# Kernel optimization log

Measured on AMD Instinct MI355X. Metric: run time of the kernel, lower is better.

## Reference

```python
import jax, jax.numpy as jnp
import numpy as np

H = 4096          # hidden_size
I = 2048          # moe_intermediate_size * n_shared_experts
SWIGLU_LIMIT = 10.0
QMAX = 127.0


def _quantize_weight(w):
    # per-output-channel symmetric int8 quantization of a float weight [out, in]
    s = jnp.maximum(jnp.max(jnp.abs(w), axis=1) / QMAX, 1e-8)      # [out]
    q = jnp.clip(jnp.round(w / s[:, None]), -QMAX, QMAX)           # int8-valued
    return q.astype(jnp.float32), s.astype(jnp.float32)


def setup_inputs() -> dict:
    key = jax.random.key(0)
    ks = jax.random.split(key, 4)
    x = jax.random.normal(ks[0], (2, 4096, H), dtype=jnp.float32)
    w_gate, s_wgate = _quantize_weight(jax.random.normal(ks[1], (I, H)) * 0.02)
    w_up, s_wup = _quantize_weight(jax.random.normal(ks[2], (I, H)) * 0.02)
    w_down, s_wdown = _quantize_weight(jax.random.normal(ks[3], (H, I)) * 0.02)
    inv_gate = jnp.ones((H,), jnp.float32)
    inv_up = jnp.ones((H,), jnp.float32)
    inv_inter = jnp.ones((I,), jnp.float32)
    return {"x": x, "w_gate": w_gate, "s_wgate": s_wgate, "w_up": w_up,
            "s_wup": s_wup, "w_down": w_down, "s_wdown": s_wdown,
            "inv_gate": inv_gate, "inv_up": inv_up, "inv_inter": inv_inter}


def _dynamic_quant(x, inv_smooth):
    # per-token symmetric int8 dynamic quant with smoothing scale
    xs = x.astype(jnp.float32) * inv_smooth                        # [T, D]
    scale = jnp.maximum(jnp.max(jnp.abs(xs), axis=-1, keepdims=True) / QMAX, 1e-8)
    q = jnp.clip(jnp.round(xs / scale), -QMAX, QMAX)
    return q, scale


def _quant_gemm(q, x_scale, w_q, w_scale):
    acc = q @ w_q.T                                                # fp32 accumulate
    return acc * x_scale * w_scale[None, :]


def reference(x, w_gate, s_wgate, w_up, s_wup, w_down, s_wdown,
              inv_gate, inv_up, inv_inter):
    orig_shape = x.shape
    x_flat = x.reshape(-1, H).astype(jnp.bfloat16)                 # [T, H]
    qg, sg = _dynamic_quant(x_flat, inv_gate)
    qu, su = _dynamic_quant(x_flat, inv_up)
    gate_out = _quant_gemm(qg, sg, w_gate, s_wgate)                # [T, I]
    up_out = _quant_gemm(qu, su, w_up, s_wup)                      # [T, I]
    inter = jax.nn.silu(gate_out) * up_out
    inter = jnp.clip(inter, -SWIGLU_LIMIT, SWIGLU_LIMIT).astype(jnp.bfloat16)
    qi, si = _dynamic_quant(inter, inv_inter)
    out = _quant_gemm(qi, si, w_down, s_wdown)                     # [T, H]
    return out.reshape(orig_shape)
```

## Files before the change

### kernel.cpp

```cpp
#include <hip/hip_runtime.h>
#include <hip/hip_bf16.h>


typedef __attribute__((ext_vector_type(4))) int i32x4;

__device__ __forceinline__ void async16(void* lds, const void* g) {
  __builtin_amdgcn_global_load_lds(
      (const __attribute__((address_space(1))) void*)g,
      (__attribute__((address_space(3))) void*)lds, 16, 0, 0);
}

__device__ __forceinline__ i32x4 mfma_i8(i32x4 a, i32x4 b, i32x4 c) {
  return __builtin_amdgcn_mfma_i32_16x16x64_i8(a, b, c, 0, 0, 0);
}

__device__ __forceinline__ float bf16_rne_f(float f) {
  unsigned u = __float_as_uint(f);
  u += 0x7fffu + ((u >> 16) & 1u);
  return __uint_as_float(u & 0xffff0000u);
}

__device__ __forceinline__ unsigned short bf16_bits(float f) {
  unsigned u = __float_as_uint(f);
  u += 0x7fffu + ((u >> 16) & 1u);
  return (unsigned short)(u >> 16);
}

__device__ __forceinline__ float bf16_to_f(unsigned short h) {
  return __uint_as_float(((unsigned)h) << 16);
}

__global__ void wconv_kernel(const float* __restrict__ w,
                             signed char* __restrict__ wq, int n) {
  int i = (blockIdx.x * 256 + threadIdx.x) * 4;
  if (i >= n) return;
  float4 f = *(const float4*)(w + i);
  signed char c[4] __attribute__((aligned(4)));
  c[0] = (signed char)(int)rintf(f.x);
  c[1] = (signed char)(int)rintf(f.y);
  c[2] = (signed char)(int)rintf(f.z);
  c[3] = (signed char)(int)rintf(f.w);
  *(int*)(wq + i) = *(const int*)c;
}

__global__ __launch_bounds__(256) void quant_x_kernel(
    const float* __restrict__ x, const float* __restrict__ invg,
    const float* __restrict__ invu, signed char* __restrict__ qg,
    signed char* __restrict__ qu, float* __restrict__ sg,
    float* __restrict__ su, int H) {
  const int t = blockIdx.x, tid = threadIdx.x;
  const float* xr = x + (size_t)t * H;
  const int c0 = tid * 16;
  float xg[16], xu[16];
  float mg = 0.f, mu = 0.f;
#pragma unroll
  for (int v = 0; v < 4; ++v) {
    float4 f = *(const float4*)(xr + c0 + v * 4);
    float4 ig = *(const float4*)(invg + c0 + v * 4);
    float4 iu = *(const float4*)(invu + c0 + v * 4);
    float b0 = bf16_rne_f(f.x), b1 = bf16_rne_f(f.y);
    float b2 = bf16_rne_f(f.z), b3 = bf16_rne_f(f.w);
    xg[v * 4 + 0] = b0 * ig.x; xg[v * 4 + 1] = b1 * ig.y;
    xg[v * 4 + 2] = b2 * ig.z; xg[v * 4 + 3] = b3 * ig.w;
    xu[v * 4 + 0] = b0 * iu.x; xu[v * 4 + 1] = b1 * iu.y;
    xu[v * 4 + 2] = b2 * iu.z; xu[v * 4 + 3] = b3 * iu.w;
#pragma unroll
    for (int j = 0; j < 4; ++j) {
      mg = fmaxf(mg, fabsf(xg[v * 4 + j]));
      mu = fmaxf(mu, fabsf(xu[v * 4 + j]));
    }
  }
#pragma unroll
  for (int off = 32; off > 0; off >>= 1) {
    mg = fmaxf(mg, __shfl_xor(mg, off));
    mu = fmaxf(mu, __shfl_xor(mu, off));
  }
  __shared__ float smg[4], smu[4];
  if ((tid & 63) == 0) { smg[tid >> 6] = mg; smu[tid >> 6] = mu; }
  __syncthreads();
  mg = fmaxf(fmaxf(smg[0], smg[1]), fmaxf(smg[2], smg[3]));
  mu = fmaxf(fmaxf(smu[0], smu[1]), fmaxf(smu[2], smu[3]));
  const float scg = fmaxf(mg / 127.0f, 1e-8f);
  const float scu = fmaxf(mu / 127.0f, 1e-8f);
  signed char og[16] __attribute__((aligned(16)));
  signed char ou[16] __attribute__((aligned(16)));
#pragma unroll
  for (int j = 0; j < 16; ++j) {
    og[j] = (signed char)(int)fminf(fmaxf(rintf(xg[j] / scg), -127.f), 127.f);
    ou[j] = (signed char)(int)fminf(fmaxf(rintf(xu[j] / scu), -127.f), 127.f);
  }
  *(i32x4*)(qg + (size_t)t * H + c0) = *(const i32x4*)og;
  *(i32x4*)(qu + (size_t)t * H + c0) = *(const i32x4*)ou;
  if (tid == 0) { sg[t] = scg; su[t] = scu; }
}

__global__ __launch_bounds__(256, 2) void gemm1_kernel(
    const signed char* __restrict__ qg, const signed char* __restrict__ qu,
    const float* __restrict__ sg, const float* __restrict__ su,
    const signed char* __restrict__ wg, const signed char* __restrict__ wu,
    const float* __restrict__ swg, const float* __restrict__ swu,
    unsigned short* __restrict__ inter, int H, int I) {
  __shared__ signed char Ag[128 * 64] __attribute__((aligned(16)));
  __shared__ signed char Au[128 * 64] __attribute__((aligned(16)));
  __shared__ signed char Bg[128 * 64] __attribute__((aligned(16)));
  __shared__ signed char Bu[128 * 64] __attribute__((aligned(16)));
  const int tid = threadIdx.x;
  const int lane = tid & 63, wave = tid >> 6;
  const int row0 = blockIdx.x * 128, col0 = blockIdx.y * 128;
  const int wm = (wave & 1) * 64, wn = (wave >> 1) * 64;
  const int mrow = lane & 15, quad = lane >> 4;

  i32x4 accG[4][4], accU[4][4];
#pragma unroll
  for (int i = 0; i < 4; ++i)
#pragma unroll
    for (int j = 0; j < 4; ++j) {
      accG[i][j] = i32x4{0, 0, 0, 0};
      accU[i][j] = i32x4{0, 0, 0, 0};
    }

  for (int kk = 0; kk < H; kk += 64) {
    __syncthreads();
#pragma unroll
    for (int p = 0; p < 2; ++p) {
      const int g = p * 256 + tid;
      const int r = g >> 2, cb = (g & 3) << 4;
      const size_t ga = (size_t)(row0 + r) * H + kk + cb;
      const size_t gb = (size_t)(col0 + r) * H + kk + cb;
      async16(&Ag[g * 16], qg + ga);
      async16(&Au[g * 16], qu + ga);
      async16(&Bg[g * 16], wg + gb);
      async16(&Bu[g * 16], wu + gb);
    }
    __syncthreads();
    i32x4 aG[4], aU[4], bG[4], bU[4];
#pragma unroll
    for (int i = 0; i < 4; ++i) {
      aG[i] = *(const i32x4*)&Ag[(wm + i * 16 + mrow) * 64 + quad * 16];
      aU[i] = *(const i32x4*)&Au[(wm + i * 16 + mrow) * 64 + quad * 16];
      bG[i] = *(const i32x4*)&Bg[(wn + i * 16 + mrow) * 64 + quad * 16];
      bU[i] = *(const i32x4*)&Bu[(wn + i * 16 + mrow) * 64 + quad * 16];
    }
#pragma unroll
    for (int i = 0; i < 4; ++i)
#pragma unroll
      for (int j = 0; j < 4; ++j) {
        accG[i][j] = mfma_i8(aG[i], bG[j], accG[i][j]);
        accU[i][j] = mfma_i8(aU[i], bU[j], accU[i][j]);
      }
  }

  float swgc[4], swuc[4];
#pragma unroll
  for (int j = 0; j < 4; ++j) {
    const int c = col0 + wn + j * 16 + mrow;
    swgc[j] = swg[c];
    swuc[j] = swu[c];
  }
#pragma unroll
  for (int i = 0; i < 4; ++i) {
#pragma unroll
    for (int r = 0; r < 4; ++r) {
      const int row = row0 + wm + i * 16 + quad * 4 + r;
      const float sgr = sg[row], sur = su[row];
#pragma unroll
      for (int j = 0; j < 4; ++j) {
        const int c = col0 + wn + j * 16 + mrow;
        const float g = (float)accG[i][j][r] * sgr * swgc[j];
        const float u = (float)accU[i][j][r] * sur * swuc[j];
        const float sig = 1.f / (1.f + expf(-g));
        float v = (g * sig) * u;
        v = fminf(fmaxf(v, -10.f), 10.f);
        inter[(size_t)row * I + c] = bf16_bits(v);
      }
    }
  }
}

__global__ __launch_bounds__(256) void quant_i_kernel(
    const unsigned short* __restrict__ inter, const float* __restrict__ invi,
    signed char* __restrict__ qi, float* __restrict__ si, int I) {
  const int t = blockIdx.x, tid = threadIdx.x;
  const unsigned short* ir = inter + (size_t)t * I;
  const int c0 = tid * 8;
  uint4 pk = *(const uint4*)(ir + c0);
  float4 i0 = *(const float4*)(invi + c0);
  float4 i1 = *(const float4*)(invi + c0 + 4);
  float xs[8];
  xs[0] = bf16_to_f(pk.x & 0xffffu) * i0.x;
  xs[1] = bf16_to_f(pk.x >> 16) * i0.y;
  xs[2] = bf16_to_f(pk.y & 0xffffu) * i0.z;
  xs[3] = bf16_to_f(pk.y >> 16) * i0.w;
  xs[4] = bf16_to_f(pk.z & 0xffffu) * i1.x;
  xs[5] = bf16_to_f(pk.z >> 16) * i1.y;
  xs[6] = bf16_to_f(pk.w & 0xffffu) * i1.z;
  xs[7] = bf16_to_f(pk.w >> 16) * i1.w;
  float m = 0.f;
#pragma unroll
  for (int j = 0; j < 8; ++j) m = fmaxf(m, fabsf(xs[j]));
#pragma unroll
  for (int off = 32; off > 0; off >>= 1) m = fmaxf(m, __shfl_xor(m, off));
  __shared__ float sm[4];
  if ((tid & 63) == 0) sm[tid >> 6] = m;
  __syncthreads();
  m = fmaxf(fmaxf(sm[0], sm[1]), fmaxf(sm[2], sm[3]));
  const float s = fmaxf(m / 127.0f, 1e-8f);
  signed char o[8] __attribute__((aligned(8)));
#pragma unroll
  for (int j = 0; j < 8; ++j)
    o[j] = (signed char)(int)fminf(fmaxf(rintf(xs[j] / s), -127.f), 127.f);
  *(unsigned long long*)(qi + (size_t)t * I + c0) = *(const unsigned long long*)o;
  if (tid == 0) si[t] = s;
}

__global__ __launch_bounds__(256, 2) void gemm2_kernel(
    const signed char* __restrict__ qi, const float* __restrict__ si,
    const signed char* __restrict__ wd, const float* __restrict__ swd,
    float* __restrict__ out, int H, int I) {
  __shared__ signed char As[128 * 64] __attribute__((aligned(16)));
  __shared__ signed char Bs[128 * 64] __attribute__((aligned(16)));
  const int tid = threadIdx.x;
  const int lane = tid & 63, wave = tid >> 6;
  const int row0 = blockIdx.x * 128, col0 = blockIdx.y * 128;
  const int wm = (wave & 1) * 64, wn = (wave >> 1) * 64;
  const int mrow = lane & 15, quad = lane >> 4;

  i32x4 acc[4][4];
#pragma unroll
  for (int i = 0; i < 4; ++i)
#pragma unroll
    for (int j = 0; j < 4; ++j) acc[i][j] = i32x4{0, 0, 0, 0};

  for (int kk = 0; kk < I; kk += 64) {
    __syncthreads();
#pragma unroll
    for (int p = 0; p < 2; ++p) {
      const int g = p * 256 + tid;
      const int r = g >> 2, cb = (g & 3) << 4;
      async16(&As[g * 16], qi + (size_t)(row0 + r) * I + kk + cb);
      async16(&Bs[g * 16], wd + (size_t)(col0 + r) * I + kk + cb);
    }
    __syncthreads();
    i32x4 a[4], b[4];
#pragma unroll
    for (int i = 0; i < 4; ++i) {
      a[i] = *(const i32x4*)&As[(wm + i * 16 + mrow) * 64 + quad * 16];
      b[i] = *(const i32x4*)&Bs[(wn + i * 16 + mrow) * 64 + quad * 16];
    }
#pragma unroll
    for (int i = 0; i < 4; ++i)
#pragma unroll
      for (int j = 0; j < 4; ++j) acc[i][j] = mfma_i8(a[i], b[j], acc[i][j]);
  }

  float swc[4];
#pragma unroll
  for (int j = 0; j < 4; ++j) swc[j] = swd[col0 + wn + j * 16 + mrow];
#pragma unroll
  for (int i = 0; i < 4; ++i) {
#pragma unroll
    for (int r = 0; r < 4; ++r) {
      const int row = row0 + wm + i * 16 + quad * 4 + r;
      const float sir = si[row];
#pragma unroll
      for (int j = 0; j < 4; ++j) {
        const int c = col0 + wn + j * 16 + mrow;
        out[(size_t)row * H + c] = (float)acc[i][j][r] * sir * swc[j];
      }
    }
  }
}

extern "C" void kernel_launch(void* const* d_in, const int* in_sizes, int n_in,
                              void* d_out, int out_size, void* d_ws,
                              size_t ws_size, hipStream_t stream) {
  const float* x = (const float*)d_in[0];
  const float* w_gate = (const float*)d_in[1];
  const float* s_wgate = (const float*)d_in[2];
  const float* w_up = (const float*)d_in[3];
  const float* s_wup = (const float*)d_in[4];
  const float* w_down = (const float*)d_in[5];
  const float* s_wdown = (const float*)d_in[6];
  const float* inv_gate = (const float*)d_in[7];
  const float* inv_up = (const float*)d_in[8];
  const float* inv_inter = (const float*)d_in[9];
  float* out = (float*)d_out;

  const int H = in_sizes[6];
  const int I = in_sizes[2];
  const int T = in_sizes[0] / H;

  char* ws = (char*)d_ws;
  size_t off = 0;
  signed char* wqg = (signed char*)(ws + off); off += (size_t)I * H;
  signed char* wqu = (signed char*)(ws + off); off += (size_t)I * H;
  signed char* wqd = (signed char*)(ws + off); off += (size_t)H * I;
  signed char* qg  = (signed char*)(ws + off); off += (size_t)T * H;
  signed char* qu  = (signed char*)(ws + off); off += (size_t)T * H;
  unsigned short* inter = (unsigned short*)(ws + off); off += (size_t)T * I * 2;
  float* sg = (float*)(ws + off); off += (size_t)T * 4;
  float* su = (float*)(ws + off); off += (size_t)T * 4;
  float* si = (float*)(ws + off); off += (size_t)T * 4;
  signed char* qi = qg;

  const int nW = I * H;
  wconv_kernel<<<nW / 1024, 256, 0, stream>>>(w_gate, wqg, nW);
  wconv_kernel<<<nW / 1024, 256, 0, stream>>>(w_up, wqu, nW);
  wconv_kernel<<<nW / 1024, 256, 0, stream>>>(w_down, wqd, nW);

  quant_x_kernel<<<T, 256, 0, stream>>>(x, inv_gate, inv_up, qg, qu, sg, su, H);

  dim3 g1(T / 128, I / 128);
  gemm1_kernel<<<g1, 256, 0, stream>>>(qg, qu, sg, su, wqg, wqu, s_wgate,
                                       s_wup, inter, H, I);

  quant_i_kernel<<<T, 256, 0, stream>>>(inter, inv_inter, qi, si, I);

  dim3 g2(T / 128, H / 128);
  gemm2_kernel<<<g2, 256, 0, stream>>>(qi, si, wqd, s_wdown, out, H, I);
}
```

Before: 612.6 us.

## Triple-buffer int8 GEMMs with larger tiles, swizzled LDS and 512-thread blocks

Both int8 GEMM kernels now use a three-stage LDS ring with async global-to-LDS loads issued two k-tiles ahead. Fine-grained vmcnt waits plus a single barrier per iteration replace the two full __syncthreads around every tile. Block tiles grow to 256x128 (gemm1) and 256x256 (gemm2) with 8 waves, and LDS rows use an XOR swizzle to reduce bank conflicts. MFMA sections are bracketed with s_setprio. The costs are much higher LDS use (about 144KB in gemm1 and 96KB in gemm2), fewer blocks in flight, and correctness now depends on the hand-tuned waitcnt counts.

```diff
diff --git a/kernel.cpp b/kernel.cpp
--- a/kernel.cpp
+++ b/kernel.cpp
@@ -29,6 +29,11 @@
 __device__ __forceinline__ float bf16_to_f(unsigned short h) {
   return __uint_as_float(((unsigned)h) << 16);
 }
+
+#define BARRIER __builtin_amdgcn_s_barrier()
+#define WAIT_VM6 asm volatile("s_waitcnt vmcnt(6) lgkmcnt(0)" ::: "memory")
+#define WAIT_VM4 asm volatile("s_waitcnt vmcnt(4) lgkmcnt(0)" ::: "memory")
+#define WAIT_VM0 asm volatile("s_waitcnt vmcnt(0) lgkmcnt(0)" ::: "memory")
 
 __global__ void wconv_kernel(const float* __restrict__ w,
                              signed char* __restrict__ wq, int n) {
@@ -94,21 +99,52 @@
   if (tid == 0) { sg[t] = scg; su[t] = scu; }
 }
 
-__global__ __launch_bounds__(256, 2) void gemm1_kernel(
+#define G1_STAGE(b, kk)                                                       \
+  {                                                                           \
+    _Pragma("unroll") for (int p = 0; p < 2; ++p) {                           \
+      const int g = p * 512 + tid;                                            \
+      const int r = g >> 2;                                                   \
+      const int c = (g & 3) ^ ((r >> 1) & 3);                                 \
+      const size_t so = (size_t)r * H + (kk) + c * 16;                        \
+      async16(&Ag[b][g * 16], qg + rowbase_a + so);                           \
+      async16(&Au[b][g * 16], qu + rowbase_a + so);                           \
+    }                                                                         \
+    {                                                                         \
+      const int r2 = tid >> 2;                                                \
+      const int c2 = (tid & 3) ^ ((r2 >> 1) & 3);                             \
+      const size_t so2 = (size_t)r2 * H + (kk) + c2 * 16;                     \
+      async16(&Bg[b][tid * 16], wg + rowbase_b + so2);                        \
+      async16(&Bu[b][tid * 16], wu + rowbase_b + so2);                        \
+    }                                                                         \
+  }
+
+__global__ __launch_bounds__(512, 2) void gemm1_kernel(
     const signed char* __restrict__ qg, const signed char* __restrict__ qu,
     const float* __restrict__ sg, const float* __restrict__ su,
     const signed char* __restrict__ wg, const signed char* __restrict__ wu,
     const float* __restrict__ swg, const float* __restrict__ swu,
     unsigned short* __restrict__ inter, int H, int I) {
-  __shared__ signed char Ag[128 * 64] __attribute__((aligned(16)));
-  __shared__ signed char Au[128 * 64] __attribute__((aligned(16)));
-  __shared__ signed char Bg[128 * 64] __attribute__((aligned(16)));
-  __shared__ signed char Bu[128 * 64] __attribute__((aligned(16)));
+  __shared__ signed char Ag[3][256 * 64] __attribute__((aligned(16)));
+  __shared__ signed char Au[3][256 * 64] __attribute__((aligned(16)));
+  __shared__ signed char Bg[3][128 * 64] __attribute__((aligned(16)));
+  __shared__ signed char Bu[3][128 * 64] __attribute__((aligned(16)));
   const int tid = threadIdx.x;
   const int lane = tid & 63, wave = tid >> 6;
-  const int row0 = blockIdx.x * 128, col0 = blockIdx.y * 128;
-  const int wm = (wave & 1) * 64, wn = (wave >> 1) * 64;
+  const int row0 = blockIdx.x * 256, col0 = blockIdx.y * 128;
+  const int wm = wave >> 1, wn = wave & 1;
   const int mrow = lane & 15, quad = lane >> 4;
+  const int NT = H >> 6;
+  const size_t rowbase_a = (size_t)row0 * H;
+  const size_t rowbase_b = (size_t)col0 * H;
+
+  int offA[4], offB[4];
+#pragma unroll
+  for (int i = 0; i < 4; ++i) {
+    const int ra = wm * 64 + i * 16 + mrow;
+    offA[i] = ra * 64 + ((quad ^ ((ra >> 1) & 3)) << 4);
+    const int rb = wn * 64 + i * 16 + mrow;
+    offB[i] = rb * 64 + ((quad ^ ((rb >> 1) & 3)) << 4);
+  }
 
   i32x4 accG[4][4], accU[4][4];
 #pragma unroll
@@ -119,28 +155,24 @@
       accU[i][j] = i32x4{0, 0, 0, 0};
     }
 
-  for (int kk = 0; kk < H; kk += 64) {
-    __syncthreads();
-#pragma unroll
-    for (int p = 0; p < 2; ++p) {
-      const int g = p * 256 + tid;
-      const int r = g >> 2, cb = (g & 3) << 4;
-      const size_t ga = (size_t)(row0 + r) * H + kk + cb;
-      const size_t gb = (size_t)(col0 + r) * H + kk + cb;
-      async16(&Ag[g * 16], qg + ga);
-      async16(&Au[g * 16], qu + ga);
-      async16(&Bg[g * 16], wg + gb);
-      async16(&Bu[g * 16], wu + gb);
-    }
-    __syncthreads();
+  G1_STAGE(0, 0);
+  G1_STAGE(1, 64);
+  asm volatile("s_waitcnt vmcnt(6)" ::: "memory");
+  BARRIER;
+
+  int bc = 0, bs = 2;
+  for (int kt = 0; kt < NT; ++kt) {
+    if (kt + 2 < NT) G1_STAGE(bs, (kt + 2) << 6);
+
     i32x4 aG[4], aU[4], bG[4], bU[4];
 #pragma unroll
     for (int i = 0; i < 4; ++i) {
-      aG[i] = *(const i32x4*)&Ag[(wm + i * 16 + mrow) * 64 + quad * 16];
-      aU[i] = *(const i32x4*)&Au[(wm + i * 16 + mrow) * 64 + quad * 16];
-      bG[i] = *(const i32x4*)&Bg[(wn + i * 16 + mrow) * 64 + quad * 16];
-      bU[i] = *(const i32x4*)&Bu[(wn + i * 16 + mrow) * 64 + quad * 16];
-    }
+      aG[i] = *(const i32x4*)(&Ag[bc][0] + offA[i]);
+      aU[i] = *(const i32x4*)(&Au[bc][0] + offA[i]);
+      bG[i] = *(const i32x4*)(&Bg[bc][0] + offB[i]);
+      bU[i] = *(const i32x4*)(&Bu[bc][0] + offB[i]);
+    }
+    __builtin_amdgcn_s_setprio(1);
 #pragma unroll
     for (int i = 0; i < 4; ++i)
 #pragma unroll
@@ -148,12 +180,23 @@
         accG[i][j] = mfma_i8(aG[i], bG[j], accG[i][j]);
         accU[i][j] = mfma_i8(aU[i], bU[j], accU[i][j]);
       }
+    __builtin_amdgcn_s_setprio(0);
+
+    if (kt + 2 < NT) {
+      WAIT_VM6;
+      BARRIER;
+    } else if (kt + 1 < NT) {
+      WAIT_VM0;
+      BARRIER;
+    }
+    bc = (bc == 2) ? 0 : bc + 1;
+    bs = (bs == 2) ? 0 : bs + 1;
   }
 
   float swgc[4], swuc[4];
 #pragma unroll
   for (int j = 0; j < 4; ++j) {
-    const int c = col0 + wn + j * 16 + mrow;
+    const int c = col0 + wn * 64 + j * 16 + mrow;
     swgc[j] = swg[c];
     swuc[j] = swu[c];
   }
@@ -161,11 +204,11 @@
   for (int i = 0; i < 4; ++i) {
 #pragma unroll
     for (int r = 0; r < 4; ++r) {
-      const int row = row0 + wm + i * 16 + quad * 4 + r;
+      const int row = row0 + wm * 64 + i * 16 + quad * 4 + r;
       const float sgr = sg[row], sur = su[row];
 #pragma unroll
       for (int j = 0; j < 4; ++j) {
-        const int c = col0 + wn + j * 16 + mrow;
+        const int c = col0 + wn * 64 + j * 16 + mrow;
         const float g = (float)accG[i][j][r] * sgr * swgc[j];
         const float u = (float)accU[i][j][r] * sur * swuc[j];
         const float sig = 1.f / (1.f + expf(-g));
@@ -213,58 +256,96 @@
   if (tid == 0) si[t] = s;
 }
 
-__global__ __launch_bounds__(256, 2) void gemm2_kernel(
+#define G2_STAGE(b, kk)                                                       \
+  {                                                                           \
+    _Pragma("unroll") for (int p = 0; p < 2; ++p) {                           \
+      const int g = p * 512 + tid;                                            \
+      const int r = g >> 2;                                                   \
+      const int c = (g & 3) ^ ((r >> 1) & 3);                                 \
+      const size_t so = (size_t)r * I + (kk) + c * 16;                        \
+      async16(&As[b][g * 16], qi + rowbase_a + so);                           \
+      async16(&Bs[b][g * 16], wd + rowbase_b + so);                           \
+    }                                                                         \
+  }
+
+__global__ __launch_bounds__(512, 2) void gemm2_kernel(
     const signed char* __restrict__ qi, const float* __restrict__ si,
     const signed char* __restrict__ wd, const float* __restrict__ swd,
     float* __restrict__ out, int H, int I) {
-  __shared__ signed char As[128 * 64] __attribute__((aligned(16)));
-  __shared__ signed char Bs[128 * 64] __attribute__((aligned(16)));
+  __shared__ signed char As[3][256 * 64] __attribute__((aligned(16)));
+  __shared__ signed char Bs[3][256 * 64] __attribute__((aligned(16)));
   const int tid = threadIdx.x;
   const int lane = tid & 63, wave = tid >> 6;
-  const int row0 = blockIdx.x * 128, col0 = blockIdx.y * 128;
-  const int wm = (wave & 1) * 64, wn = (wave >> 1) * 64;
+  const int row0 = blockIdx.x * 256, col0 = blockIdx.y * 256;
+  const int wm = wave >> 2, wn = wave & 3;
   const int mrow = lane & 15, quad = lane >> 4;
-
-  i32x4 acc[4][4];
-#pragma unroll
-  for (int i = 0; i < 4; ++i)
+  const int NT = I >> 6;
+  const size_t rowbase_a = (size_t)row0 * I;
+  const size_t rowbase_b = (size_t)col0 * I;
+
+  int offA[8], offB[4];
+#pragma unroll
+  for (int i = 0; i < 8; ++i) {
+    const int ra = wm * 128 + i * 16 + mrow;
+    offA[i] = ra * 64 + ((quad ^ ((ra >> 1) & 3)) << 4);
+  }
+#pragma unroll
+  for (int j = 0; j < 4; ++j) {
+    const int rb = wn * 64 + j * 16 + mrow;
+    offB[j] = rb * 64 + ((quad ^ ((rb >> 1) & 3)) << 4);
+  }
+
+  i32x4 acc[8][4];
+#pragma unroll
+  for (int i = 0; i < 8; ++i)
 #pragma unroll
     for (int j = 0; j < 4; ++j) acc[i][j] = i32x4{0, 0, 0, 0};
 
-  for (int kk = 0; kk < I; kk += 64) {
-    __syncthreads();
-#pragma unroll
-    for (int p = 0; p < 2; ++p) {
-      const int g = p * 256 + tid;
-      const int r = g >> 2, cb = (g & 3) << 4;
-      async16(&As[g * 16], qi + (size_t)(row0 + r) * I + kk + cb);
-      async16(&Bs[g * 16], wd + (size_t)(col0 + r) * I + kk + cb);
-    }
-    __syncthreads();
-    i32x4 a[4], b[4];
-#pragma unroll
-    for (int i = 0; i < 4; ++i) {
-      a[i] = *(const i32x4*)&As[(wm + i * 16 + mrow) * 64 + quad * 16];
-      b[i] = *(const i32x4*)&Bs[(wn + i * 16 + mrow) * 64 + quad * 16];
-    }
-#pragma unroll
-    for (int i = 0; i < 4; ++i)
+  G2_STAGE(0, 0);
+  G2_STAGE(1, 64);
+  asm volatile("s_waitcnt vmcnt(4)" ::: "memory");
+  BARRIER;
+
+  int bc = 0, bs = 2;
+  for (int kt = 0; kt < NT; ++kt) {
+    if (kt + 2 < NT) G2_STAGE(bs, (kt + 2) << 6);
+
+    i32x4 a[8], b[4];
+#pragma unroll
+    for (int i = 0; i < 8; ++i) a[i] = *(const i32x4*)(&As[bc][0] + offA[i]);
+#pragma unroll
+    for (int j = 0; j < 4; ++j) b[j] = *(const i32x4*)(&Bs[bc][0] + offB[j]);
+
+    __builtin_amdgcn_s_setprio(1);
+#pragma unroll
+    for (int i = 0; i < 8; ++i)
 #pragma unroll
       for (int j = 0; j < 4; ++j) acc[i][j] = mfma_i8(a[i], b[j], acc[i][j]);
+    __builtin_amdgcn_s_setprio(0);
+
+    if (kt + 2 < NT) {
+      WAIT_VM4;
+      BARRIER;
+    } else if (kt + 1 < NT) {
+      WAIT_VM0;
+      BARRIER;
+    }
+    bc = (bc == 2) ? 0 : bc + 1;
+    bs = (bs == 2) ? 0 : bs + 1;
   }
 
   float swc[4];
 #pragma unroll
-  for (int j = 0; j < 4; ++j) swc[j] = swd[col0 + wn + j * 16 + mrow];
-#pragma unroll
-  for (int i = 0; i < 4; ++i) {
+  for (int j = 0; j < 4; ++j) swc[j] = swd[col0 + wn * 64 + j * 16 + mrow];
+#pragma unroll
+  for (int i = 0; i < 8; ++i) {
 #pragma unroll
     for (int r = 0; r < 4; ++r) {
-      const int row = row0 + wm + i * 16 + quad * 4 + r;
+      const int row = row0 + wm * 128 + i * 16 + quad * 4 + r;
       const float sir = si[row];
 #pragma unroll
       for (int j = 0; j < 4; ++j) {
-        const int c = col0 + wn + j * 16 + mrow;
+        const int c = col0 + wn * 64 + j * 16 + mrow;
         out[(size_t)row * H + c] = (float)acc[i][j][r] * sir * swc[j];
       }
     }
@@ -310,12 +391,12 @@
 
   quant_x_kernel<<<T, 256, 0, stream>>>(x, inv_gate, inv_up, qg, qu, sg, su, H);
 
-  dim3 g1(T / 128, I / 128);
-  gemm1_kernel<<<g1, 256, 0, stream>>>(qg, qu, sg, su, wqg, wqu, s_wgate,
+  dim3 g1(T / 256, I / 128);
+  gemm1_kernel<<<g1, 512, 0, stream>>>(qg, qu, sg, su, wqg, wqu, s_wgate,
                                        s_wup, inter, H, I);
 
   quant_i_kernel<<<T, 256, 0, stream>>>(inter, inv_inter, qi, si, I);
 
-  dim3 g2(T / 128, H / 128);
-  gemm2_kernel<<<g2, 256, 0, stream>>>(qi, si, wqd, s_wdown, out, H, I);
-}
+  dim3 g2(T / 256, H / 256);
+  gemm2_kernel<<<g2, 512, 0, stream>>>(qi, si, wqd, s_wdown, out, H, I);
+}
```

After: 648.1 us. 5.8% more time.

## Double-buffer LDS tiles with async prefetch and XOR-swizzle in both int8 GEMMs

Applied to the files above, without the earlier changes.

Both GEMM kernels now use two LDS buffers and issue the global-to-LDS loads for the next K tile before computing on the current one. They wait with explicit vmcnt counts and barriers instead of two __syncthreads per iteration, so load latency can overlap with MFMA work. The LDS layout is also XOR-swizzled on 16-byte chunks to reduce bank conflicts on the fragment reads. The cost is doubled LDS use: 64 KB per block in gemm1, which may limit the two-blocks-per-CU occupancy target. The hand-written waitcnt values also have to match the exact number of loads issued per stage.

```diff
diff --git a/kernel.cpp b/kernel.cpp
--- a/kernel.cpp
+++ b/kernel.cpp
@@ -29,6 +29,12 @@
 __device__ __forceinline__ float bf16_to_f(unsigned short h) {
   return __uint_as_float(((unsigned)h) << 16);
 }
+
+#define BARRIER __builtin_amdgcn_s_barrier()
+#define LGKM0 asm volatile("s_waitcnt lgkmcnt(0)" ::: "memory")
+#define WAIT_VM8 asm volatile("s_waitcnt vmcnt(8)" ::: "memory")
+#define WAIT_VM4 asm volatile("s_waitcnt vmcnt(4)" ::: "memory")
+#define WAIT_VM0 asm volatile("s_waitcnt vmcnt(0)" ::: "memory")
 
 __global__ void wconv_kernel(const float* __restrict__ w,
                              signed char* __restrict__ wq, int n) {
@@ -94,21 +100,46 @@
   if (tid == 0) { sg[t] = scg; su[t] = scu; }
 }
 
+#define G1_STAGE(b, kk)                                                       \
+  {                                                                           \
+    _Pragma("unroll") for (int p = 0; p < 2; ++p) {                           \
+      const int g_ = p * 256 + tid;                                           \
+      const int r_ = g_ >> 2;                                                 \
+      const int c_ = (g_ & 3) ^ ((r_ >> 1) & 3);                              \
+      const size_t ga_ = (size_t)(row0 + r_) * H + (kk) + c_ * 16;            \
+      const size_t gb_ = (size_t)(col0 + r_) * H + (kk) + c_ * 16;            \
+      async16(&Ag[b][g_ * 16], qg + ga_);                                     \
+      async16(&Au[b][g_ * 16], qu + ga_);                                     \
+      async16(&Bg[b][g_ * 16], wg + gb_);                                     \
+      async16(&Bu[b][g_ * 16], wu + gb_);                                     \
+    }                                                                         \
+  }
+
 __global__ __launch_bounds__(256, 2) void gemm1_kernel(
     const signed char* __restrict__ qg, const signed char* __restrict__ qu,
     const float* __restrict__ sg, const float* __restrict__ su,
     const signed char* __restrict__ wg, const signed char* __restrict__ wu,
     const float* __restrict__ swg, const float* __restrict__ swu,
     unsigned short* __restrict__ inter, int H, int I) {
-  __shared__ signed char Ag[128 * 64] __attribute__((aligned(16)));
-  __shared__ signed char Au[128 * 64] __attribute__((aligned(16)));
-  __shared__ signed char Bg[128 * 64] __attribute__((aligned(16)));
-  __shared__ signed char Bu[128 * 64] __attribute__((aligned(16)));
+  __shared__ signed char Ag[2][128 * 64] __attribute__((aligned(16)));
+  __shared__ signed char Au[2][128 * 64] __attribute__((aligned(16)));
+  __shared__ signed char Bg[2][128 * 64] __attribute__((aligned(16)));
+  __shared__ signed char Bu[2][128 * 64] __attribute__((aligned(16)));
   const int tid = threadIdx.x;
   const int lane = tid & 63, wave = tid >> 6;
   const int row0 = blockIdx.x * 128, col0 = blockIdx.y * 128;
   const int wm = (wave & 1) * 64, wn = (wave >> 1) * 64;
   const int mrow = lane & 15, quad = lane >> 4;
+  const int NT = H >> 6;
+
+  int offA[4], offB[4];
+#pragma unroll
+  for (int i = 0; i < 4; ++i) {
+    const int ra = wm + i * 16 + mrow;
+    offA[i] = ra * 64 + ((quad ^ ((ra >> 1) & 3)) << 4);
+    const int rb = wn + i * 16 + mrow;
+    offB[i] = rb * 64 + ((quad ^ ((rb >> 1) & 3)) << 4);
+  }
 
   i32x4 accG[4][4], accU[4][4];
 #pragma unroll
@@ -119,27 +150,25 @@
       accU[i][j] = i32x4{0, 0, 0, 0};
     }
 
-  for (int kk = 0; kk < H; kk += 64) {
-    __syncthreads();
-#pragma unroll
-    for (int p = 0; p < 2; ++p) {
-      const int g = p * 256 + tid;
-      const int r = g >> 2, cb = (g & 3) << 4;
-      const size_t ga = (size_t)(row0 + r) * H + kk + cb;
-      const size_t gb = (size_t)(col0 + r) * H + kk + cb;
-      async16(&Ag[g * 16], qg + ga);
-      async16(&Au[g * 16], qu + ga);
-      async16(&Bg[g * 16], wg + gb);
-      async16(&Bu[g * 16], wu + gb);
-    }
-    __syncthreads();
+  G1_STAGE(0, 0);
+
+  int cur = 0;
+  for (int kt = 0; kt < NT; ++kt) {
+    if (kt + 1 < NT) {
+      G1_STAGE(cur ^ 1, (kt + 1) << 6);
+      WAIT_VM8;
+    } else {
+      WAIT_VM0;
+    }
+    BARRIER;
+
     i32x4 aG[4], aU[4], bG[4], bU[4];
 #pragma unroll
     for (int i = 0; i < 4; ++i) {
-      aG[i] = *(const i32x4*)&Ag[(wm + i * 16 + mrow) * 64 + quad * 16];
-      aU[i] = *(const i32x4*)&Au[(wm + i * 16 + mrow) * 64 + quad * 16];
-      bG[i] = *(const i32x4*)&Bg[(wn + i * 16 + mrow) * 64 + quad * 16];
-      bU[i] = *(const i32x4*)&Bu[(wn + i * 16 + mrow) * 64 + quad * 16];
+      aG[i] = *(const i32x4*)(&Ag[cur][0] + offA[i]);
+      aU[i] = *(const i32x4*)(&Au[cur][0] + offA[i]);
+      bG[i] = *(const i32x4*)(&Bg[cur][0] + offB[i]);
+      bU[i] = *(const i32x4*)(&Bu[cur][0] + offB[i]);
     }
 #pragma unroll
     for (int i = 0; i < 4; ++i)
@@ -148,6 +177,10 @@
         accG[i][j] = mfma_i8(aG[i], bG[j], accG[i][j]);
         accU[i][j] = mfma_i8(aU[i], bU[j], accU[i][j]);
       }
+
+    LGKM0;
+    BARRIER;
+    cur ^= 1;
   }
 
   float swgc[4], swuc[4];
@@ -213,17 +246,40 @@
   if (tid == 0) si[t] = s;
 }
 
+#define G2_STAGE(b, kk)                                                       \
+  {                                                                           \
+    _Pragma("unroll") for (int p = 0; p < 2; ++p) {                           \
+      const int g_ = p * 256 + tid;                                           \
+      const int r_ = g_ >> 2;                                                 \
+      const int c_ = (g_ & 3) ^ ((r_ >> 1) & 3);                              \
+      async16(&As[b][g_ * 16],                                                \
+              qi + (size_t)(row0 + r_) * I + (kk) + c_ * 16);                 \
+      async16(&Bs[b][g_ * 16],                                                \
+              wd + (size_t)(col0 + r_) * I + (kk) + c_ * 16);                 \
+    }                                                                         \
+  }
+
 __global__ __launch_bounds__(256, 2) void gemm2_kernel(
     const signed char* __restrict__ qi, const float* __restrict__ si,
     const signed char* __restrict__ wd, const float* __restrict__ swd,
     float* __restrict__ out, int H, int I) {
-  __shared__ signed char As[128 * 64] __attribute__((aligned(16)));
-  __shared__ signed char Bs[128 * 64] __attribute__((aligned(16)));
+  __shared__ signed char As[2][128 * 64] __attribute__((aligned(16)));
+  __shared__ signed char Bs[2][128 * 64] __attribute__((aligned(16)));
   const int tid = threadIdx.x;
   const int lane = tid & 63, wave = tid >> 6;
   const int row0 = blockIdx.x * 128, col0 = blockIdx.y * 128;
   const int wm = (wave & 1) * 64, wn = (wave >> 1) * 64;
   const int mrow = lane & 15, quad = lane >> 4;
+  const int NT = I >> 6;
+
+  int offA[4], offB[4];
+#pragma unroll
+  for (int i = 0; i < 4; ++i) {
+    const int ra = wm + i * 16 + mrow;
+    offA[i] = ra * 64 + ((quad ^ ((ra >> 1) & 3)) << 4);
+    const int rb = wn + i * 16 + mrow;
+    offB[i] = rb * 64 + ((quad ^ ((rb >> 1) & 3)) << 4);
+  }
 
   i32x4 acc[4][4];
 #pragma unroll
@@ -231,26 +287,32 @@
 #pragma unroll
     for (int j = 0; j < 4; ++j) acc[i][j] = i32x4{0, 0, 0, 0};
 
-  for (int kk = 0; kk < I; kk += 64) {
-    __syncthreads();
-#pragma unroll
-    for (int p = 0; p < 2; ++p) {
-      const int g = p * 256 + tid;
-      const int r = g >> 2, cb = (g & 3) << 4;
-      async16(&As[g * 16], qi + (size_t)(row0 + r) * I + kk + cb);
-      async16(&Bs[g * 16], wd + (size_t)(col0 + r) * I + kk + cb);
-    }
-    __syncthreads();
+  G2_STAGE(0, 0);
+
+  int cur = 0;
+  for (int kt = 0; kt < NT; ++kt) {
+    if (kt + 1 < NT) {
+      G2_STAGE(cur ^ 1, (kt + 1) << 6);
+      WAIT_VM4;
+    } else {
+      WAIT_VM0;
+    }
+    BARRIER;
+
     i32x4 a[4], b[4];
 #pragma unroll
     for (int i = 0; i < 4; ++i) {
-      a[i] = *(const i32x4*)&As[(wm + i * 16 + mrow) * 64 + quad * 16];
-      b[i] = *(const i32x4*)&Bs[(wn + i * 16 + mrow) * 64 + quad * 16];
+      a[i] = *(const i32x4*)(&As[cur][0] + offA[i]);
+      b[i] = *(const i32x4*)(&Bs[cur][0] + offB[i]);
     }
 #pragma unroll
     for (int i = 0; i < 4; ++i)
 #pragma unroll
       for (int j = 0; j < 4; ++j) acc[i][j] = mfma_i8(a[i], b[j], acc[i][j]);
+
+    LGKM0;
+    BARRIER;
+    cur ^= 1;
   }
 
   float swc[4];
```

After: 612.1 us. Within noise of the previous version (-0.1%).
